# Performance work log

Measured on AMD Instinct MI355X. Metric: run time of the kernel, lower is better.

## Reference

```python
import jax, jax.numpy as jnp
import numpy as np

B, L, D, N = 2, 2048, 1024, 16
H = D // N  # head dim 64
MASK_FILL = -100000000.0  # torch code uses -1e8 for non-fp16


def sinusoidal_pos(seq_len, dim):
    # interleaved (sin, cos) table, shape (seq_len, dim); identical per head
    inv_freq = 1.0 / (10000.0 ** (jnp.arange(0, dim, 2, dtype=jnp.float32) / dim))
    ang = jnp.arange(seq_len, dtype=jnp.float32)[:, None] * inv_freq[None, :]
    return jnp.stack([jnp.sin(ang), jnp.cos(ang)], axis=-1).reshape(seq_len, dim)


def apply_rope(x, pos_emb):
    # x: (b, n, l, h); pos_emb: (l, h) interleaved sin/cos
    cos = jnp.repeat(pos_emb[..., 1::2], 2, axis=-1)  # (l, h)
    sin = jnp.repeat(pos_emb[..., ::2], 2, axis=-1)
    x2 = jnp.stack([-x[..., 1::2], x[..., ::2]], axis=-1).reshape(x.shape)
    return x * cos + x2 * sin


def setup_inputs() -> dict:
    key = jax.random.key(0)
    ks = jax.random.split(key, 12)
    inp = {
        "q": jax.random.normal(ks[0], (B, L, D), dtype=jnp.float32),
        "k": jax.random.normal(ks[1], (B, L, D), dtype=jnp.float32),
        "v": jax.random.normal(ks[2], (B, L, D), dtype=jnp.float32),
        "mask": jax.random.bernoulli(ks[3], 0.3, (B, L)),  # True = masked
    }
    s = 0.02
    for i, name in enumerate(["q", "k", "v", "o"]):
        inp[f"W{name}"] = jax.random.normal(ks[4 + i], (D, D), dtype=jnp.float32) * s
        inp[f"b{name}"] = jax.random.normal(ks[8 + i], (D,), dtype=jnp.float32) * s
    return inp


def reference(q, k, v, mask, Wq, bq, Wk, bk, Wv, bv, Wo, bo):
    # projections (torch Linear: x @ W^T + b) and head split -> (b, n, l, h)
    def split_heads(x):
        return x.reshape(B, L, N, H).transpose(0, 2, 1, 3)

    qw = split_heads(q @ Wq.T + bq)
    kw = split_heads(k @ Wk.T + bk)
    vw = split_heads(v @ Wv.T + bv)

    pos = sinusoidal_pos(L, H)
    qw = apply_rope(qw, pos)
    kw = apply_rope(kw, pos)

    # NOTE: original scales by sqrt(hidden_dim), not sqrt(head_dim)
    scores = jnp.einsum("bnlh,bnph->bnlp", qw, kw) / np.sqrt(D).astype(np.float32)
    scores = jnp.where(mask[:, None, None, :], MASK_FILL, scores)
    attn = jax.nn.softmax(scores, axis=-1)  # dropout is identity in eval

    out = jnp.einsum("bnlp,bnph->bnlh", attn, vw)  # (b, n, l, h)
    out = out.transpose(0, 2, 1, 3).reshape(B, L, D)
    return out @ Wo.T + bo
```

## Files before the change

kernel.cpp:

```cpp
#include <hip/hip_runtime.h>
#include <stdint.h>

#define L_SEQ 2048
#define DMODEL 1024
#define NHEAD 16
#define HDIM 64
#define BATCH 2

typedef __attribute__((ext_vector_type(8))) short bf16x8;
typedef __attribute__((ext_vector_type(4))) float f32x4;

#define MFMA(a, b, c) __builtin_amdgcn_mfma_f32_16x16x32_bf16((a), (b), (c), 0, 0, 0)

#if __has_builtin(__builtin_amdgcn_exp2f)
#define EXP2(x) __builtin_amdgcn_exp2f(x)
#else
#define EXP2(x) exp2f(x)
#endif

#if __has_builtin(__builtin_amdgcn_wave_barrier)
#define WAVE_FENCE() __builtin_amdgcn_wave_barrier()
#else
#define WAVE_FENCE() __syncthreads()
#endif

#define QSCALE 0.04508422f

__device__ __forceinline__ unsigned short f2bf(float f) {
    return (unsigned short)((__float_as_uint(f) + 0x8000u) >> 16);
}
__device__ __forceinline__ float bf2f(unsigned short h) {
    return __uint_as_float(((unsigned int)h) << 16);
}
__device__ __forceinline__ unsigned int pkbf(float a, float b) {
    return __builtin_amdgcn_perm(__float_as_uint(b) + 0x8000u,
                                 __float_as_uint(a) + 0x8000u, 0x07060302u);
}
__device__ __forceinline__ void gl2lds16(const unsigned short* g, unsigned short* l) {
    __builtin_amdgcn_global_load_lds(
        (const __attribute__((address_space(1))) void*)g,
        (__attribute__((address_space(3))) void*)l, 16, 0, 0);
}

__global__ void prep_kernel(
    const float* __restrict__ q, const float* __restrict__ k, const float* __restrict__ v,
    const float* __restrict__ wq, const float* __restrict__ wk, const float* __restrict__ wv,
    const float* __restrict__ Wo, const int* __restrict__ mask,
    unsigned short* __restrict__ xb, unsigned short* __restrict__ wb,
    unsigned short* __restrict__ whi, unsigned short* __restrict__ wlo,
    float2* __restrict__ ropetab, unsigned long long* __restrict__ mbits)
{
    const int y = blockIdx.y, x = blockIdx.x, tid = threadIdx.x;
    if (y < 6) {
        const float* src = (y == 0) ? q : (y == 1) ? k : (y == 2) ? v
                         : (y == 3) ? wq : (y == 4) ? wk : wv;
        unsigned short* dst = (y < 3) ? xb + (size_t)y * 4194304
                                      : wb + (size_t)(y - 3) * 1048576;
        const int n = (y < 3) ? 4194304 : 1048576;
        const int i = (x * 256 + tid) * 8;
        if (i >= n) return;
        const float4 a = *(const float4*)(src + i);
        const float4 b = *(const float4*)(src + i + 4);
        uint4 u;
        u.x = pkbf(a.x, a.y); u.y = pkbf(a.z, a.w);
        u.z = pkbf(b.x, b.y); u.w = pkbf(b.z, b.w);
        *(uint4*)(dst + i) = u;
    } else if (y == 6) {
        const int i = (x * 256 + tid) * 4;
        if (i >= DMODEL * DMODEL) return;
        const float4 vv = *(const float4*)(Wo + i);
        const float f[4] = {vv.x, vv.y, vv.z, vv.w};
        union { unsigned short s[4]; uint2 u; } h, l;
#pragma unroll
        for (int r = 0; r < 4; ++r) {
            h.s[r] = f2bf(f[r]);
            l.s[r] = f2bf(f[r] - bf2f(h.s[r]));
        }
        *(uint2*)&whi[i] = h.u;
        *(uint2*)&wlo[i] = l.u;
    } else {
        if (x < 512) {
            const int idx = x * 256 + tid;
            const int l = idx >> 6, h = idx & 63;
            const float invf = powf(10000.0f, -(float)(h & 62) * (1.0f / 64.0f));
            float sn, cs;
            sincosf((float)l * invf, &sn, &cs);
            ropetab[idx] = make_float2(cs, sn);
        } else if (x < 528) {
            const int w = (x - 512) * 4 + (tid >> 6);
            const unsigned long long bal = __ballot(mask[w * 64 + (tid & 63)] != 0);
            if ((tid & 63) == 0) mbits[w] = bal;
        }
    }
}

__global__ __launch_bounds__(256) void qkv_kernel(
    const unsigned short* __restrict__ Xb, const unsigned short* __restrict__ Wb,
    const float* __restrict__ bq, const float* __restrict__ bk, const float* __restrict__ bv,
    const float2* __restrict__ ropetab,
    unsigned short* __restrict__ Qd, unsigned short* __restrict__ Kd,
    unsigned short* __restrict__ Vd)
{
    const int id = blockIdx.x;
    const int bx = id / 96, rem = id % 96;
    const int z = rem >> 5, by = rem & 31;

    const unsigned short* X = Xb + (size_t)z * (BATCH * L_SEQ * DMODEL);
    const unsigned short* W = Wb + (size_t)z * (DMODEL * DMODEL);
    const float* bias = (z == 0) ? bq : (z == 1) ? bk : bv;

    __shared__ __align__(16) unsigned short As[128 * 64];
    __shared__ __align__(16) unsigned short Bs[128 * 64];

    const int tid  = threadIdx.x;
    const int wave = tid >> 6, lane = tid & 63;
    const int ml = lane & 15, kq = lane >> 4;
    const int m0 = by * 128, n0 = bx * 128;
    const int wm = (wave & 1) * 64, wn = (wave >> 1) * 64;

    f32x4 acc[4][4];
#pragma unroll
    for (int i = 0; i < 4; ++i)
#pragma unroll
        for (int j = 0; j < 4; ++j) acc[i][j] = (f32x4){0.f, 0.f, 0.f, 0.f};

    const int prow = wave * 32 + (lane >> 3);
    const int pch  = (lane & 7) ^ ((lane >> 3) & 7);
    const unsigned short* gA = X + (size_t)(m0 + prow) * DMODEL + pch * 8;
    const unsigned short* gB = W + (size_t)(n0 + prow) * DMODEL + pch * 8;
    unsigned short* lA = As + wave * 2048;
    unsigned short* lB = Bs + wave * 2048;

    for (int kc = 0; kc < DMODEL; kc += 64) {
#pragma unroll
        for (int qq = 0; qq < 4; ++qq) {
            gl2lds16(gA + kc + (size_t)qq * 8 * DMODEL, lA + qq * 512);
            gl2lds16(gB + kc + (size_t)qq * 8 * DMODEL, lB + qq * 512);
        }
        __syncthreads();

        bf16x8 af[2][4], bfv[2][4];
#pragma unroll
        for (int ks = 0; ks < 2; ++ks)
#pragma unroll
            for (int i = 0; i < 4; ++i) {
                const int Ra = wm + i * 16 + ml;
                af[ks][i] = *(const bf16x8*)&As[Ra * 64 + (((ks * 4 + kq) ^ (Ra & 7)) << 3)];
                const int Rb = wn + i * 16 + ml;
                bfv[ks][i] = *(const bf16x8*)&Bs[Rb * 64 + (((ks * 4 + kq) ^ (Rb & 7)) << 3)];
            }
#pragma unroll
        for (int ks = 0; ks < 2; ++ks)
#pragma unroll
            for (int i = 0; i < 4; ++i)
#pragma unroll
                for (int j = 0; j < 4; ++j)
                    acc[i][j] = MFMA(af[ks][i], bfv[ks][j], acc[i][j]);
        __syncthreads();
    }

    if (z < 2) {
        unsigned short* dst = (z == 0) ? Qd : Kd;
        const float osc = (z == 0) ? QSCALE : 1.0f;
#pragma unroll
        for (int jt = 0; jt < 4; ++jt) {
            const int col = n0 + wn + jt * 16 + ml;
            const float bv = bias[col];
            const int nh = col >> 6, hh = col & 63;
            const int odd = hh & 1;
#pragma unroll
            for (int it = 0; it < 4; ++it) {
#pragma unroll
                for (int r = 0; r < 4; ++r) {
                    const int row = m0 + wm + it * 16 + kq * 4 + r;
                    const int bb = row >> 11, ll = row & 2047;
                    const float v = acc[it][jt][r] + bv;
                    const float partner = __shfl_xor(v, 1);
                    const float2 cs = ropetab[ll * 64 + hh];
                    const float res = odd ? fmaf(v, cs.x, partner * cs.y)
                                          : fmaf(v, cs.x, -partner * cs.y);
                    dst[(((size_t)(bb * NHEAD + nh) * L_SEQ + ll) << 6) + hh] = f2bf(res * osc);
                }
            }
        }
    } else {
#pragma unroll
        for (int jt = 0; jt < 4; ++jt) {
            const int col = n0 + wn + jt * 16 + ml;
            const float bv = bias[col];
            const int nh = col >> 6, hh = col & 63;
#pragma unroll
            for (int it = 0; it < 4; ++it) {
                const int rb = m0 + wm + it * 16 + kq * 4;
                const int bb = rb >> 11, ll = rb & 2047;
                uint2 pk;
                pk.x = pkbf(acc[it][jt][0] + bv, acc[it][jt][1] + bv);
                pk.y = pkbf(acc[it][jt][2] + bv, acc[it][jt][3] + bv);
                *(uint2*)&Vd[(((size_t)bb * NHEAD + nh) * HDIM + hh) * L_SEQ + ll] = pk;
            }
        }
    }
}

__global__ __launch_bounds__(256) void attn_kernel(
    const unsigned short* __restrict__ Qr, const unsigned short* __restrict__ Kr,
    const unsigned short* __restrict__ Vt, const unsigned long long* __restrict__ mbits,
    unsigned short* __restrict__ AOhi, unsigned short* __restrict__ AOlo)
{
    __shared__ __align__(16) unsigned short Ks[2][64 * 64];
    __shared__ __align__(16) unsigned short Vs[2][64 * 64];
    __shared__ __align__(16) unsigned short Ps[4][16 * 64];

    const int tid  = threadIdx.x;
    const int wave = tid >> 6, lane = tid & 63;
    const int ml = lane & 15, kq = lane >> 4;

    const int id = blockIdx.x;
    const int xcd = id & 7, slot = id >> 3;
    const int bh = xcd * 4 + (slot & 3);
    const int qb = slot >> 2;
    const int b = bh >> 4, nh = bh & 15;
    const int q0 = qb * 64;
    const int wq = wave * 16;

    const unsigned short* Qp = Qr + (size_t)bh * L_SEQ * HDIM;
    const unsigned short* Kp = Kr + (size_t)bh * L_SEQ * HDIM;
    const unsigned short* Vp = Vt + (size_t)bh * HDIM * L_SEQ;

    bf16x8 qf0 = *(const bf16x8*)(Qp + (size_t)(q0 + wq + ml) * HDIM + kq * 8);
    bf16x8 qf1 = *(const bf16x8*)(Qp + (size_t)(q0 + wq + ml) * HDIM + 32 + kq * 8);

    float li = 0.f;
    f32x4 o[4];
#pragma unroll
    for (int ht = 0; ht < 4; ++ht) o[ht] = (f32x4){0.f, 0.f, 0.f, 0.f};

    unsigned short* Pw = Ps[wave];

    const int srow8 = lane >> 3;
    const int sch   = (lane & 7) ^ srow8;
    const unsigned short* gK = Kp + (size_t)(wave * 16 + srow8) * HDIM + sch * 8;
    const unsigned short* gV = Vp + (size_t)(wave * 16 + srow8) * L_SEQ + sch * 8;

#define STAGE(kt, bf)                                                          \
    do {                                                                       \
        gl2lds16(gK + (size_t)((kt) * 64) * HDIM, &Ks[bf][(wave * 16) * 64]);  \
        gl2lds16(gK + (size_t)((kt) * 64 + 8) * HDIM,                          \
                 &Ks[bf][(wave * 16 + 8) * 64]);                               \
        gl2lds16(gV + (kt) * 64, &Vs[bf][(wave * 16) * 64]);                   \
        gl2lds16(gV + (size_t)8 * L_SEQ + (kt) * 64,                           \
                 &Vs[bf][(wave * 16 + 8) * 64]);                               \
    } while (0)

    STAGE(0, 0);

    for (int kt = 0; kt < L_SEQ / 64; ++kt) {
        const int buf = kt & 1;
        __syncthreads();
        if (kt + 1 < L_SEQ / 64) STAGE(kt + 1, buf ^ 1);

        const unsigned short* Kb = Ks[buf];
        const unsigned short* Vb = Vs[buf];
        const unsigned long long mw = mbits[b * 32 + kt];

        f32x4 st[4];
#pragma unroll
        for (int nt = 0; nt < 4; ++nt) {
            const int R = nt * 16 + ml;
            const bf16x8 kf0 = *(const bf16x8*)&Kb[R * 64 + ((kq ^ (R & 7)) << 3)];
            const bf16x8 kf1 = *(const bf16x8*)&Kb[R * 64 + (((4 + kq) ^ (R & 7)) << 3)];
            f32x4 c = (f32x4){0.f, 0.f, 0.f, 0.f};
            c = MFMA(kf0, qf0, c);
            c = MFMA(kf1, qf1, c);
            st[nt] = c;
        }

#pragma unroll
        for (int nt = 0; nt < 4; ++nt) {
            const unsigned int nib = ((unsigned int)(mw >> (nt * 16 + kq * 4))) & 0xFu;
            float p[4];
#pragma unroll
            for (int r = 0; r < 4; ++r) {
                const float e = EXP2(st[nt][r]);
                p[r] = (nib & (1u << r)) ? 0.f : e;
                li += p[r];
            }
            uint2 pk;
            pk.x = pkbf(p[0], p[1]);
            pk.y = pkbf(p[2], p[3]);
            const int ck = nt * 2 + (kq >> 1);
            *(uint2*)&Pw[ml * 64 + ((ck ^ (ml & 7)) << 3) + (kq & 1) * 4] = pk;
        }
        WAVE_FENCE();

        const bf16x8 pf0 = *(const bf16x8*)&Pw[ml * 64 + ((kq ^ (ml & 7)) << 3)];
        const bf16x8 pf1 = *(const bf16x8*)&Pw[ml * 64 + (((4 + kq) ^ (ml & 7)) << 3)];
#pragma unroll
        for (int ht = 0; ht < 4; ++ht) {
            const int R = ht * 16 + ml;
            const bf16x8 vf0 = *(const bf16x8*)&Vb[R * 64 + ((kq ^ (R & 7)) << 3)];
            const bf16x8 vf1 = *(const bf16x8*)&Vb[R * 64 + (((4 + kq) ^ (R & 7)) << 3)];
            o[ht] = MFMA(vf0, pf0, o[ht]);
            o[ht] = MFMA(vf1, pf1, o[ht]);
        }
        WAVE_FENCE();
    }
#undef STAGE

    li += __shfl_xor(li, 16);
    li += __shfl_xor(li, 32);
    const float inv = 1.f / li;

    const int qr = lane >> 2, quarter = lane & 3;
    const size_t gbase = ((size_t)b * L_SEQ + q0 + wq + qr) * DMODEL + nh * 64 + quarter * 16;
    const int rc0 = (quarter * 2) ^ (qr & 7), rc1 = (quarter * 2 + 1) ^ (qr & 7);

#pragma unroll
    for (int ht = 0; ht < 4; ++ht) {
        uint2 pk;
        pk.x = pkbf(o[ht][0] * inv, o[ht][1] * inv);
        pk.y = pkbf(o[ht][2] * inv, o[ht][3] * inv);
        const int ck = ht * 2 + (kq >> 1);
        *(uint2*)&Pw[ml * 64 + ((ck ^ (ml & 7)) << 3) + (kq & 1) * 4] = pk;
    }
    WAVE_FENCE();
    {
        const uint4 d0 = *(const uint4*)&Pw[qr * 64 + (rc0 << 3)];
        const uint4 d1 = *(const uint4*)&Pw[qr * 64 + (rc1 << 3)];
        *(uint4*)&AOhi[gbase]     = d0;
        *(uint4*)&AOhi[gbase + 8] = d1;
    }
    WAVE_FENCE();
#pragma unroll
    for (int ht = 0; ht < 4; ++ht) {
        float lo[4];
#pragma unroll
        for (int r = 0; r < 4; ++r) {
            const float v = o[ht][r] * inv;
            const float hf = __uint_as_float((__float_as_uint(v) + 0x8000u) & 0xffff0000u);
            lo[r] = v - hf;
        }
        uint2 pk;
        pk.x = pkbf(lo[0], lo[1]);
        pk.y = pkbf(lo[2], lo[3]);
        const int ck = ht * 2 + (kq >> 1);
        *(uint2*)&Pw[ml * 64 + ((ck ^ (ml & 7)) << 3) + (kq & 1) * 4] = pk;
    }
    WAVE_FENCE();
    {
        const uint4 d0 = *(const uint4*)&Pw[qr * 64 + (rc0 << 3)];
        const uint4 d1 = *(const uint4*)&Pw[qr * 64 + (rc1 << 3)];
        *(uint4*)&AOlo[gbase]     = d0;
        *(uint4*)&AOlo[gbase + 8] = d1;
    }
}

__global__ __launch_bounds__(256) void oproj_kernel(
    const unsigned short* __restrict__ Ahi_g, const unsigned short* __restrict__ Alo_g,
    const unsigned short* __restrict__ Whi_g, const unsigned short* __restrict__ Wlo_g,
    const float* __restrict__ bias, float* __restrict__ out)
{
    const int id = blockIdx.x;
    const int bx = id >> 5, by = id & 31;

    __shared__ __align__(16) unsigned short Ah[128 * 32], Al[128 * 32];
    __shared__ __align__(16) unsigned short Bh[128 * 32], Bl[128 * 32];

    const int tid  = threadIdx.x;
    const int wave = tid >> 6, lane = tid & 63;
    const int ml = lane & 15, kq = lane >> 4;
    const int m0 = by * 128, n0 = bx * 128;
    const int wm = (wave & 1) * 64, wn = (wave >> 1) * 64;

    f32x4 acc[4][4];
#pragma unroll
    for (int i = 0; i < 4; ++i)
#pragma unroll
        for (int j = 0; j < 4; ++j) acc[i][j] = (f32x4){0.f, 0.f, 0.f, 0.f};

    const int prow = wave * 32 + (lane >> 2);
    const int pch  = (lane & 3) ^ ((lane >> 3) & 3);
    const unsigned short* gAh = Ahi_g + (size_t)(m0 + prow) * DMODEL + pch * 8;
    const unsigned short* gAl = Alo_g + (size_t)(m0 + prow) * DMODEL + pch * 8;
    const unsigned short* gBh = Whi_g + (size_t)(n0 + prow) * DMODEL + pch * 8;
    const unsigned short* gBl = Wlo_g + (size_t)(n0 + prow) * DMODEL + pch * 8;
    unsigned short* lAh = Ah + wave * 1024;
    unsigned short* lAl = Al + wave * 1024;
    unsigned short* lBh = Bh + wave * 1024;
    unsigned short* lBl = Bl + wave * 1024;

    for (int kc = 0; kc < DMODEL; kc += 32) {
#pragma unroll
        for (int qq = 0; qq < 2; ++qq) {
            const size_t go = kc + (size_t)qq * 16 * DMODEL;
            gl2lds16(gAh + go, lAh + qq * 512);
            gl2lds16(gAl + go, lAl + qq * 512);
            gl2lds16(gBh + go, lBh + qq * 512);
            gl2lds16(gBl + go, lBl + qq * 512);
        }
        __syncthreads();

        bf16x8 ah[4], al[4], bh_[4], bl_[4];
#pragma unroll
        for (int i = 0; i < 4; ++i) {
            const int Ra = wm + i * 16 + ml;
            const int sa = Ra * 32 + ((kq ^ ((Ra >> 1) & 3)) << 3);
            ah[i] = *(const bf16x8*)&Ah[sa];
            al[i] = *(const bf16x8*)&Al[sa];
            const int Rb = wn + i * 16 + ml;
            const int sb = Rb * 32 + ((kq ^ ((Rb >> 1) & 3)) << 3);
            bh_[i] = *(const bf16x8*)&Bh[sb];
            bl_[i] = *(const bf16x8*)&Bl[sb];
        }
#pragma unroll
        for (int i = 0; i < 4; ++i)
#pragma unroll
            for (int j = 0; j < 4; ++j) {
                acc[i][j] = MFMA(ah[i], bh_[j], acc[i][j]);
                acc[i][j] = MFMA(al[i], bh_[j], acc[i][j]);
                acc[i][j] = MFMA(ah[i], bl_[j], acc[i][j]);
            }
        __syncthreads();
    }

#pragma unroll
    for (int jt = 0; jt < 4; ++jt) {
        const int col = n0 + wn + jt * 16 + ml;
        const float bv = bias[col];
#pragma unroll
        for (int it = 0; it < 4; ++it)
#pragma unroll
            for (int r = 0; r < 4; ++r) {
                const int row = m0 + wm + it * 16 + kq * 4 + r;
                out[(size_t)row * DMODEL + col] = acc[it][jt][r] + bv;
            }
    }
}

extern "C" void kernel_launch(void* const* d_in, const int* in_sizes, int n_in,
                              void* d_out, int out_size, void* d_ws, size_t ws_size,
                              hipStream_t stream)
{
    (void)in_sizes; (void)n_in; (void)out_size; (void)ws_size;
    const float* q    = (const float*)d_in[0];
    const float* k    = (const float*)d_in[1];
    const float* v    = (const float*)d_in[2];
    const int*   mask = (const int*)d_in[3];
    const float* Wq   = (const float*)d_in[4];
    const float* bq   = (const float*)d_in[5];
    const float* Wk   = (const float*)d_in[6];
    const float* bk   = (const float*)d_in[7];
    const float* Wv   = (const float*)d_in[8];
    const float* bv   = (const float*)d_in[9];
    const float* Wo   = (const float*)d_in[10];
    const float* bo   = (const float*)d_in[11];
    float* out = (float*)d_out;

    const size_t HE = (size_t)BATCH * NHEAD * L_SEQ * HDIM;
    const size_t DD = (size_t)DMODEL * DMODEL;
    unsigned short* Xb   = (unsigned short*)d_ws;
    unsigned short* Wb   = Xb + 3 * HE;
    unsigned short* Qr   = Wb + 3 * DD;
    unsigned short* Kr   = Qr + HE;
    unsigned short* Vt   = Kr + HE;
    unsigned short* Whi  = Vt + HE;
    unsigned short* Wlo  = Whi + DD;
    unsigned long long* mbits = (unsigned long long*)(Wlo + DD);
    float2* ropetab = (float2*)(mbits + BATCH * L_SEQ / 64);
    unsigned short* AOhi = Xb;
    unsigned short* AOlo = Xb + HE;

    prep_kernel<<<dim3(2048, 8), dim3(256), 0, stream>>>(
        q, k, v, Wq, Wk, Wv, Wo, mask, Xb, Wb, Whi, Wlo, ropetab, mbits);

    qkv_kernel<<<dim3(768), dim3(256), 0, stream>>>(Xb, Wb, bq, bk, bv, ropetab, Qr, Kr, Vt);

    attn_kernel<<<dim3(1024), dim3(256), 0, stream>>>(Qr, Kr, Vt, mbits, AOhi, AOlo);

    oproj_kernel<<<dim3(256), dim3(256), 0, stream>>>(AOhi, AOlo, Whi, Wlo, bo, out);
}
```

Measured before the change: 267.5 us.

## Double per-wave query rows in attention and halve oproj N-tile

The attention kernel now has each wave handle 32 query rows (two 16-row tiles) instead of 16, so every K/V tile staged into LDS is reused across twice as many queries. The grid is halved to 512 blocks and the per-wave P scratch is doubled. Separately, the output projection tile shrinks from 128x128 to 128x64, doubling its block count to 512 for better CU occupancy. The trade-off is more registers per attention wave and half as many attention blocks, versus less K/V traffic.

New measurement: 257.3 us. 3.8% less time.

```diff
diff --git a/kernel.cpp b/kernel.cpp
--- a/kernel.cpp
+++ b/kernel.cpp
@@ -209,7 +209,7 @@
 {
     __shared__ __align__(16) unsigned short Ks[2][64 * 64];
     __shared__ __align__(16) unsigned short Vs[2][64 * 64];
-    __shared__ __align__(16) unsigned short Ps[4][16 * 64];
+    __shared__ __align__(16) unsigned short Ps[4][32 * 64];
 
     const int tid  = threadIdx.x;
     const int wave = tid >> 6, lane = tid & 63;
@@ -220,20 +220,26 @@
     const int bh = xcd * 4 + (slot & 3);
     const int qb = slot >> 2;
     const int b = bh >> 4, nh = bh & 15;
-    const int q0 = qb * 64;
-    const int wq = wave * 16;
+    const int q0 = qb * 128;
+    const int wq = wave * 32;
 
     const unsigned short* Qp = Qr + (size_t)bh * L_SEQ * HDIM;
     const unsigned short* Kp = Kr + (size_t)bh * L_SEQ * HDIM;
     const unsigned short* Vp = Vt + (size_t)bh * HDIM * L_SEQ;
 
-    bf16x8 qf0 = *(const bf16x8*)(Qp + (size_t)(q0 + wq + ml) * HDIM + kq * 8);
-    bf16x8 qf1 = *(const bf16x8*)(Qp + (size_t)(q0 + wq + ml) * HDIM + 32 + kq * 8);
-
-    float li = 0.f;
-    f32x4 o[4];
-#pragma unroll
-    for (int ht = 0; ht < 4; ++ht) o[ht] = (f32x4){0.f, 0.f, 0.f, 0.f};
+    bf16x8 qf[2][2];
+#pragma unroll
+    for (int qt = 0; qt < 2; ++qt)
+#pragma unroll
+        for (int c = 0; c < 2; ++c)
+            qf[qt][c] = *(const bf16x8*)(Qp + (size_t)(q0 + wq + qt * 16 + ml) * HDIM + c * 32 + kq * 8);
+
+    float li[2] = {0.f, 0.f};
+    f32x4 o[2][4];
+#pragma unroll
+    for (int qt = 0; qt < 2; ++qt)
+#pragma unroll
+        for (int ht = 0; ht < 4; ++ht) o[qt][ht] = (f32x4){0.f, 0.f, 0.f, 0.f};
 
     unsigned short* Pw = Ps[wave];
 
@@ -263,93 +269,125 @@
         const unsigned short* Vb = Vs[buf];
         const unsigned long long mw = mbits[b * 32 + kt];
 
-        f32x4 st[4];
+        f32x4 st[2][4];
 #pragma unroll
         for (int nt = 0; nt < 4; ++nt) {
             const int R = nt * 16 + ml;
             const bf16x8 kf0 = *(const bf16x8*)&Kb[R * 64 + ((kq ^ (R & 7)) << 3)];
             const bf16x8 kf1 = *(const bf16x8*)&Kb[R * 64 + (((4 + kq) ^ (R & 7)) << 3)];
-            f32x4 c = (f32x4){0.f, 0.f, 0.f, 0.f};
-            c = MFMA(kf0, qf0, c);
-            c = MFMA(kf1, qf1, c);
-            st[nt] = c;
-        }
-
-#pragma unroll
-        for (int nt = 0; nt < 4; ++nt) {
-            const unsigned int nib = ((unsigned int)(mw >> (nt * 16 + kq * 4))) & 0xFu;
-            float p[4];
-#pragma unroll
-            for (int r = 0; r < 4; ++r) {
-                const float e = EXP2(st[nt][r]);
-                p[r] = (nib & (1u << r)) ? 0.f : e;
-                li += p[r];
-            }
-            uint2 pk;
-            pk.x = pkbf(p[0], p[1]);
-            pk.y = pkbf(p[2], p[3]);
-            const int ck = nt * 2 + (kq >> 1);
-            *(uint2*)&Pw[ml * 64 + ((ck ^ (ml & 7)) << 3) + (kq & 1) * 4] = pk;
+#pragma unroll
+            for (int qt = 0; qt < 2; ++qt) {
+                f32x4 c = (f32x4){0.f, 0.f, 0.f, 0.f};
+                c = MFMA(kf0, qf[qt][0], c);
+                c = MFMA(kf1, qf[qt][1], c);
+                st[qt][nt] = c;
+            }
+        }
+
+        unsigned int nib[4];
+#pragma unroll
+        for (int nt = 0; nt < 4; ++nt)
+            nib[nt] = ((unsigned int)(mw >> (nt * 16 + kq * 4))) & 0xFu;
+#pragma unroll
+        for (int qt = 0; qt < 2; ++qt) {
+#pragma unroll
+            for (int nt = 0; nt < 4; ++nt) {
+                float p[4];
+#pragma unroll
+                for (int r = 0; r < 4; ++r) {
+                    const float e = EXP2(st[qt][nt][r]);
+                    p[r] = (nib[nt] & (1u << r)) ? 0.f : e;
+                    li[qt] += p[r];
+                }
+                uint2 pk;
+                pk.x = pkbf(p[0], p[1]);
+                pk.y = pkbf(p[2], p[3]);
+                const int row = qt * 16 + ml;
+                const int ck = nt * 2 + (kq >> 1);
+                *(uint2*)&Pw[row * 64 + ((ck ^ (ml & 7)) << 3) + (kq & 1) * 4] = pk;
+            }
         }
         WAVE_FENCE();
 
-        const bf16x8 pf0 = *(const bf16x8*)&Pw[ml * 64 + ((kq ^ (ml & 7)) << 3)];
-        const bf16x8 pf1 = *(const bf16x8*)&Pw[ml * 64 + (((4 + kq) ^ (ml & 7)) << 3)];
+        bf16x8 pf[2][2];
+#pragma unroll
+        for (int qt = 0; qt < 2; ++qt) {
+            const int row = qt * 16 + ml;
+            pf[qt][0] = *(const bf16x8*)&Pw[row * 64 + ((kq ^ (ml & 7)) << 3)];
+            pf[qt][1] = *(const bf16x8*)&Pw[row * 64 + (((4 + kq) ^ (ml & 7)) << 3)];
+        }
 #pragma unroll
         for (int ht = 0; ht < 4; ++ht) {
             const int R = ht * 16 + ml;
             const bf16x8 vf0 = *(const bf16x8*)&Vb[R * 64 + ((kq ^ (R & 7)) << 3)];
             const bf16x8 vf1 = *(const bf16x8*)&Vb[R * 64 + (((4 + kq) ^ (R & 7)) << 3)];
-            o[ht] = MFMA(vf0, pf0, o[ht]);
-            o[ht] = MFMA(vf1, pf1, o[ht]);
+#pragma unroll
+            for (int qt = 0; qt < 2; ++qt) {
+                o[qt][ht] = MFMA(vf0, pf[qt][0], o[qt][ht]);
+                o[qt][ht] = MFMA(vf1, pf[qt][1], o[qt][ht]);
+            }
         }
         WAVE_FENCE();
     }
 #undef STAGE
 
-    li += __shfl_xor(li, 16);
-    li += __shfl_xor(li, 32);
-    const float inv = 1.f / li;
+#pragma unroll
+    for (int qt = 0; qt < 2; ++qt) {
+        li[qt] += __shfl_xor(li[qt], 16);
+        li[qt] += __shfl_xor(li[qt], 32);
+    }
+    const float inv[2] = {1.f / li[0], 1.f / li[1]};
 
     const int qr = lane >> 2, quarter = lane & 3;
-    const size_t gbase = ((size_t)b * L_SEQ + q0 + wq + qr) * DMODEL + nh * 64 + quarter * 16;
     const int rc0 = (quarter * 2) ^ (qr & 7), rc1 = (quarter * 2 + 1) ^ (qr & 7);
 
 #pragma unroll
-    for (int ht = 0; ht < 4; ++ht) {
-        uint2 pk;
-        pk.x = pkbf(o[ht][0] * inv, o[ht][1] * inv);
-        pk.y = pkbf(o[ht][2] * inv, o[ht][3] * inv);
-        const int ck = ht * 2 + (kq >> 1);
-        *(uint2*)&Pw[ml * 64 + ((ck ^ (ml & 7)) << 3) + (kq & 1) * 4] = pk;
-    }
+    for (int qt = 0; qt < 2; ++qt)
+#pragma unroll
+        for (int ht = 0; ht < 4; ++ht) {
+            uint2 pk;
+            pk.x = pkbf(o[qt][ht][0] * inv[qt], o[qt][ht][1] * inv[qt]);
+            pk.y = pkbf(o[qt][ht][2] * inv[qt], o[qt][ht][3] * inv[qt]);
+            const int row = qt * 16 + ml;
+            const int ck = ht * 2 + (kq >> 1);
+            *(uint2*)&Pw[row * 64 + ((ck ^ (ml & 7)) << 3) + (kq & 1) * 4] = pk;
+        }
     WAVE_FENCE();
-    {
-        const uint4 d0 = *(const uint4*)&Pw[qr * 64 + (rc0 << 3)];
-        const uint4 d1 = *(const uint4*)&Pw[qr * 64 + (rc1 << 3)];
+#pragma unroll
+    for (int qt = 0; qt < 2; ++qt) {
+        const size_t gbase = ((size_t)b * L_SEQ + q0 + wq + qt * 16 + qr) * DMODEL
+                             + nh * 64 + quarter * 16;
+        const uint4 d0 = *(const uint4*)&Pw[(qt * 16 + qr) * 64 + (rc0 << 3)];
+        const uint4 d1 = *(const uint4*)&Pw[(qt * 16 + qr) * 64 + (rc1 << 3)];
         *(uint4*)&AOhi[gbase]     = d0;
         *(uint4*)&AOhi[gbase + 8] = d1;
     }
     WAVE_FENCE();
 #pragma unroll
-    for (int ht = 0; ht < 4; ++ht) {
-        float lo[4];
-#pragma unroll
-        for (int r = 0; r < 4; ++r) {
-            const float v = o[ht][r] * inv;
-            const float hf = __uint_as_float((__float_as_uint(v) + 0x8000u) & 0xffff0000u);
-            lo[r] = v - hf;
-        }
-        uint2 pk;
-        pk.x = pkbf(lo[0], lo[1]);
-        pk.y = pkbf(lo[2], lo[3]);
-        const int ck = ht * 2 + (kq >> 1);
-        *(uint2*)&Pw[ml * 64 + ((ck ^ (ml & 7)) << 3) + (kq & 1) * 4] = pk;
-    }
+    for (int qt = 0; qt < 2; ++qt)
+#pragma unroll
+        for (int ht = 0; ht < 4; ++ht) {
+            float lo[4];
+#pragma unroll
+            for (int r = 0; r < 4; ++r) {
+                const float v = o[qt][ht][r] * inv[qt];
+                const float hf = __uint_as_float((__float_as_uint(v) + 0x8000u) & 0xffff0000u);
+                lo[r] = v - hf;
+            }
+            uint2 pk;
+            pk.x = pkbf(lo[0], lo[1]);
+            pk.y = pkbf(lo[2], lo[3]);
+            const int row = qt * 16 + ml;
+            const int ck = ht * 2 + (kq >> 1);
+            *(uint2*)&Pw[row * 64 + ((ck ^ (ml & 7)) << 3) + (kq & 1) * 4] = pk;
+        }
     WAVE_FENCE();
-    {
-        const uint4 d0 = *(const uint4*)&Pw[qr * 64 + (rc0 << 3)];
-        const uint4 d1 = *(const uint4*)&Pw[qr * 64 + (rc1 << 3)];
+#pragma unroll
+    for (int qt = 0; qt < 2; ++qt) {
+        const size_t gbase = ((size_t)b * L_SEQ + q0 + wq + qt * 16 + qr) * DMODEL
+                             + nh * 64 + quarter * 16;
+        const uint4 d0 = *(const uint4*)&Pw[(qt * 16 + qr) * 64 + (rc0 << 3)];
+        const uint4 d1 = *(const uint4*)&Pw[(qt * 16 + qr) * 64 + (rc1 << 3)];
         *(uint4*)&AOlo[gbase]     = d0;
         *(uint4*)&AOlo[gbase + 8] = d1;
     }
@@ -361,33 +399,35 @@
     const float* __restrict__ bias, float* __restrict__ out)
 {
     const int id = blockIdx.x;
-    const int bx = id >> 5, by = id & 31;
+    const int bxn = id >> 5, by = id & 31;
 
     __shared__ __align__(16) unsigned short Ah[128 * 32], Al[128 * 32];
-    __shared__ __align__(16) unsigned short Bh[128 * 32], Bl[128 * 32];
+    __shared__ __align__(16) unsigned short Bh[64 * 32],  Bl[64 * 32];
 
     const int tid  = threadIdx.x;
     const int wave = tid >> 6, lane = tid & 63;
     const int ml = lane & 15, kq = lane >> 4;
-    const int m0 = by * 128, n0 = bx * 128;
-    const int wm = (wave & 1) * 64, wn = (wave >> 1) * 64;
-
-    f32x4 acc[4][4];
+    const int m0 = by * 128, n0 = bxn * 64;
+    const int wm = (wave & 1) * 64, wn = (wave >> 1) * 32;
+
+    f32x4 acc[4][2];
 #pragma unroll
     for (int i = 0; i < 4; ++i)
 #pragma unroll
-        for (int j = 0; j < 4; ++j) acc[i][j] = (f32x4){0.f, 0.f, 0.f, 0.f};
-
-    const int prow = wave * 32 + (lane >> 2);
-    const int pch  = (lane & 3) ^ ((lane >> 3) & 3);
-    const unsigned short* gAh = Ahi_g + (size_t)(m0 + prow) * DMODEL + pch * 8;
-    const unsigned short* gAl = Alo_g + (size_t)(m0 + prow) * DMODEL + pch * 8;
-    const unsigned short* gBh = Whi_g + (size_t)(n0 + prow) * DMODEL + pch * 8;
-    const unsigned short* gBl = Wlo_g + (size_t)(n0 + prow) * DMODEL + pch * 8;
+        for (int j = 0; j < 2; ++j) acc[i][j] = (f32x4){0.f, 0.f, 0.f, 0.f};
+
+    const int rl  = lane >> 2;
+    const int pch = (lane & 3) ^ ((lane >> 3) & 3);
+    const int prowA = wave * 32 + rl;
+    const int prowB = wave * 16 + rl;
+    const unsigned short* gAh = Ahi_g + (size_t)(m0 + prowA) * DMODEL + pch * 8;
+    const unsigned short* gAl = Alo_g + (size_t)(m0 + prowA) * DMODEL + pch * 8;
+    const unsigned short* gBh = Whi_g + (size_t)(n0 + prowB) * DMODEL + pch * 8;
+    const unsigned short* gBl = Wlo_g + (size_t)(n0 + prowB) * DMODEL + pch * 8;
     unsigned short* lAh = Ah + wave * 1024;
     unsigned short* lAl = Al + wave * 1024;
-    unsigned short* lBh = Bh + wave * 1024;
-    unsigned short* lBl = Bl + wave * 1024;
+    unsigned short* lBh = Bh + wave * 512;
+    unsigned short* lBl = Bl + wave * 512;
 
     for (int kc = 0; kc < DMODEL; kc += 32) {
 #pragma unroll
@@ -395,27 +435,30 @@
             const size_t go = kc + (size_t)qq * 16 * DMODEL;
             gl2lds16(gAh + go, lAh + qq * 512);
             gl2lds16(gAl + go, lAl + qq * 512);
-            gl2lds16(gBh + go, lBh + qq * 512);
-            gl2lds16(gBl + go, lBl + qq * 512);
-        }
+        }
+        gl2lds16(gBh + kc, lBh);
+        gl2lds16(gBl + kc, lBl);
         __syncthreads();
 
-        bf16x8 ah[4], al[4], bh_[4], bl_[4];
+        bf16x8 ah[4], al[4], bh_[2], bl_[2];
 #pragma unroll
         for (int i = 0; i < 4; ++i) {
             const int Ra = wm + i * 16 + ml;
             const int sa = Ra * 32 + ((kq ^ ((Ra >> 1) & 3)) << 3);
             ah[i] = *(const bf16x8*)&Ah[sa];
             al[i] = *(const bf16x8*)&Al[sa];
-            const int Rb = wn + i * 16 + ml;
+        }
+#pragma unroll
+        for (int j = 0; j < 2; ++j) {
+            const int Rb = wn + j * 16 + ml;
             const int sb = Rb * 32 + ((kq ^ ((Rb >> 1) & 3)) << 3);
-            bh_[i] = *(const bf16x8*)&Bh[sb];
-            bl_[i] = *(const bf16x8*)&Bl[sb];
+            bh_[j] = *(const bf16x8*)&Bh[sb];
+            bl_[j] = *(const bf16x8*)&Bl[sb];
         }
 #pragma unroll
         for (int i = 0; i < 4; ++i)
 #pragma unroll
-            for (int j = 0; j < 4; ++j) {
+            for (int j = 0; j < 2; ++j) {
                 acc[i][j] = MFMA(ah[i], bh_[j], acc[i][j]);
                 acc[i][j] = MFMA(al[i], bh_[j], acc[i][j]);
                 acc[i][j] = MFMA(ah[i], bl_[j], acc[i][j]);
@@ -424,7 +467,7 @@
     }
 
 #pragma unroll
-    for (int jt = 0; jt < 4; ++jt) {
+    for (int jt = 0; jt < 2; ++jt) {
         const int col = n0 + wn + jt * 16 + ml;
         const float bv = bias[col];
 #pragma unroll
@@ -475,7 +518,7 @@
 
     qkv_kernel<<<dim3(768), dim3(256), 0, stream>>>(Xb, Wb, bq, bk, bv, ropetab, Qr, Kr, Vt);
 
-    attn_kernel<<<dim3(1024), dim3(256), 0, stream>>>(Qr, Kr, Vt, mbits, AOhi, AOlo);
-
-    oproj_kernel<<<dim3(256), dim3(256), 0, stream>>>(AOhi, AOlo, Whi, Wlo, bo, out);
-}
+    attn_kernel<<<dim3(512), dim3(256), 0, stream>>>(Qr, Kr, Vt, mbits, AOhi, AOlo);
+
+    oproj_kernel<<<dim3(512), dim3(256), 0, stream>>>(AOhi, AOlo, Whi, Wlo, bo, out);
+}
```
